# Kernel optimization log

Measured on AMD Instinct MI355X. Metric: run time of the kernel, lower is better.

## Reference

```python
import jax, jax.numpy as jnp
import numpy as np


def _cal_similarity(query, respond):
    # query: [B, n1, d], respond: [B, n2, d]
    # scores[b, c, q, r] = <query[b, q], respond[c, r]>
    scores = jnp.einsum('bqd,crd->bcqr', query, respond)  # [B, B, n1, n2]
    # max over respond tokens, mean over query tokens -> [B, B]
    return scores.max(axis=-1).mean(axis=-1)


def _ce_with_arange_labels(logits):
    # cross-entropy with labels = arange(B), mean reduction
    logp = jax.nn.log_softmax(logits, axis=-1)
    return -jnp.mean(jnp.diagonal(logp))


def setup_inputs() -> dict:
    key = jax.random.key(0)
    k1, k2 = jax.random.split(key)
    B, n1, n2, d = 96, 196, 77, 512
    image_out = jax.random.normal(k1, (B, n1, d), dtype=jnp.float32)
    text_out = jax.random.normal(k2, (B, n2, d), dtype=jnp.float32)
    return {"image_out": image_out, "text_out": text_out}


def reference(image_out, text_out):
    i2t = _cal_similarity(image_out, text_out)  # [B, B]
    t2i = _cal_similarity(text_out, image_out)  # [B, B]
    return 0.5 * (_ce_with_arange_labels(i2t) + _ce_with_arange_labels(t2i))
```

## Files before the change

kernel.cpp:

```cpp
#include <hip/hip_runtime.h>
#include <math.h>

#define BB 96
#define N1 196
#define N2 77
#define DD 512

#define IMGN (BB * N1 * DD)
#define TXTN (BB * N2 * DD)

#define ATILES 13
#define NTILES 24
#define BUFH (NTILES * 512)

typedef _Float16 f16x8 __attribute__((ext_vector_type(8)));
typedef float f4v __attribute__((ext_vector_type(4)));

typedef unsigned int __attribute__((address_space(1))) as1_uint;
typedef unsigned int __attribute__((address_space(3))) as3_uint;

__device__ __forceinline__ void gload_lds16(const void* g, void* l) {
    __builtin_amdgcn_global_load_lds((const as1_uint*)g, (as3_uint*)l, 16, 0, 0);
}

__global__ void convert_kernel(const float* __restrict__ img,
                               const float* __restrict__ txt,
                               _Float16* __restrict__ dst) {
    int i = (blockIdx.x * blockDim.x + threadIdx.x) * 4;
    if (i >= IMGN + TXTN) return;
    const float* src = (i < IMGN) ? (img + i) : (txt + (i - IMGN));
    float4 v = *(const float4*)src;
    union { _Float16 h[4]; uint2 u; } o;
    o.h[0] = (_Float16)v.x; o.h[1] = (_Float16)v.y;
    o.h[2] = (_Float16)v.z; o.h[3] = (_Float16)v.w;
    *(uint2*)(dst + i) = o.u;
}

template <int SG0, int NS, int H>
__device__ __forceinline__ void compute_sub(const f16x8* __restrict__ fr,
                                            f4v* __restrict__ acc, int lane) {
    f16x8 b[5];
#pragma unroll
    for (int ct = 0; ct < 5; ++ct)
        b[ct] = fr[(ATILES + H * 5 + ct) * 64 + lane];
#pragma unroll
    for (int i = 0; i < NS; ++i) {
        f16x8 a = fr[(SG0 + i) * 64 + lane];
#pragma unroll
        for (int ct = 0; ct < 5; ++ct)
            acc[i * 5 + ct] = __builtin_amdgcn_mfma_f32_16x16x32_f16(
                a, b[ct], acc[i * 5 + ct], 0, 0, 0);
    }
}

template <int SG0, int NS, int H>
__device__ __forceinline__ void reduce_phase1(const f4v* __restrict__ acc,
                                              int g, int lq, int lm,
                                              float* __restrict__ rp,
                                              float* __restrict__ cp) {
    float colm[5];
#pragma unroll
    for (int ct = 0; ct < 5; ++ct) colm[ct] = -INFINITY;
#pragma unroll
    for (int i = 0; i < NS; ++i) {
        const int s = SG0 + i;
        float rowm[4] = {-INFINITY, -INFINITY, -INFINITY, -INFINITY};
        bool rows_ok = (s != 12) || (lq == 0);
#pragma unroll
        for (int ct = 0; ct < 5; ++ct) {
            f4v a = acc[i * 5 + ct];
            bool col_ok = (ct != 4) || (lm < N2 - 64);
            float cm = fmaxf(fmaxf(a[0], a[1]), fmaxf(a[2], a[3]));
            colm[ct] = fmaxf(colm[ct], rows_ok ? cm : -INFINITY);
#pragma unroll
            for (int r = 0; r < 4; ++r)
                rowm[r] = fmaxf(rowm[r], col_ok ? a[r] : -INFINITY);
        }
#pragma unroll
        for (int r = 0; r < 4; ++r) {
            float m = rowm[r];
            m = fmaxf(m, __shfl_xor(m, 1));
            m = fmaxf(m, __shfl_xor(m, 2));
            m = fmaxf(m, __shfl_xor(m, 4));
            m = fmaxf(m, __shfl_xor(m, 8));
            if (lm == 0) rp[H * 208 + s * 16 + lq * 4 + r] = m;
        }
    }
#pragma unroll
    for (int ct = 0; ct < 5; ++ct) {
        float m = colm[ct];
        m = fmaxf(m, __shfl_xor(m, 16));
        m = fmaxf(m, __shfl_xor(m, 32));
        if (lq == 0) cp[g * 160 + H * 80 + ct * 16 + lm] = m;
    }
}

template <bool PRE>
__global__ __launch_bounds__(256, 2) void sim_mfma_kernel(
    const float* __restrict__ imgF, const float* __restrict__ txtF,
    const _Float16* __restrict__ h16,
    float* __restrict__ i2t, float* __restrict__ t2i)
{
    const int id  = blockIdx.x;
    const int xcd = id & 7;
    const int lid = id >> 3;
    const int w   = lid % 48;
    const int btq = lid / 48;
    const int btp = btq * 4 + (w & 3);
    const int bi  = xcd * 12 + (w >> 2);
    const int bt0 = btp * 2;

    const int tid = threadIdx.x;
    const int wave = tid >> 6, lane = tid & 63;
    const int lm = lane & 15;
    const int lq = lane >> 4;
    const int g = wave >> 1;

    __shared__ __align__(16) _Float16 lds[3 * BUFH];
    float* scratch = (float*)(lds + 2 * BUFH);
    float* rp   = scratch;
    float* cp   = scratch + 416;
    float* sws  = scratch + 736;
    float* scol = scratch + 740;

    int off[6];
    const float* fsrc[6];
#pragma unroll
    for (int j = 0; j < 6; ++j) {
        const int T = 4 * j + wave;
        int o;
        bool isA = true;
        if (T < ATILES) {
            int q = T * 16 + lm; q = q > (N1 - 1) ? (N1 - 1) : q;
            o = (bi * N1 + q) * DD + lq * 8;
        } else if (T < 23) {
            isA = false;
            int ct = T - ATILES;
            int bt = bt0 + (ct >= 5);
            int r = (ct % 5) * 16 + lm; r = r > (N2 - 1) ? (N2 - 1) : r;
            o = (bt * N2 + r) * DD + lq * 8;
        } else {
            o = lq * 8;
        }
        if constexpr (PRE) {
            off[j] = isA ? o : (IMGN + o);
        } else {
            off[j] = o;
            fsrc[j] = isA ? imgF : txtF;
        }
    }

    auto stage = [&](int kc, int b) {
        const int k0 = kc * 32;
#pragma unroll
        for (int j = 0; j < 6; ++j)
            gload_lds16(h16 + off[j] + k0,
                        lds + (b * NTILES + 4 * j + wave) * 512);
    };

    f4v acc[35];
#pragma unroll
    for (int i = 0; i < 35; ++i) acc[i] = (f4v){0.f, 0.f, 0.f, 0.f};

    auto do_compute = [&](const f16x8* fr) {
        if (wave == 0)      compute_sub<0, 7, 0>(fr, acc, lane);
        else if (wave == 1) compute_sub<0, 7, 1>(fr, acc, lane);
        else if (wave == 2) compute_sub<7, 6, 0>(fr, acc, lane);
        else                compute_sub<7, 6, 1>(fr, acc, lane);
    };

    if constexpr (PRE) {
        stage(0, 0);
        stage(1, 1);
#pragma unroll 1
        for (int kc = 0; kc < 16; ++kc) {
            if (kc < 14) {
                stage(kc + 2, (kc + 2) % 3);
                asm volatile("s_waitcnt vmcnt(12)" ::: "memory");
            } else if (kc == 14) {
                asm volatile("s_waitcnt vmcnt(6)" ::: "memory");
            } else {
                asm volatile("s_waitcnt vmcnt(0)" ::: "memory");
            }
            __builtin_amdgcn_s_barrier();
            asm volatile("" ::: "memory");
            do_compute((const f16x8*)(lds + (kc % 3) * BUFH));
            asm volatile("" ::: "memory");
            __builtin_amdgcn_s_barrier();
        }
    } else {
#pragma unroll 1
        for (int kc = 0; kc < 16; ++kc) {
            __syncthreads();
            const int k0 = kc * 32;
#pragma unroll
            for (int j = 0; j < 6; ++j) {
                const int T = 4 * j + wave;
                if (T < 23) {
                    float4 v0 = *(const float4*)(fsrc[j] + off[j] + k0);
                    float4 v1 = *(const float4*)(fsrc[j] + off[j] + k0 + 4);
                    union { f16x8 f; uint4 u; } o;
                    o.f[0] = (_Float16)v0.x; o.f[1] = (_Float16)v0.y;
                    o.f[2] = (_Float16)v0.z; o.f[3] = (_Float16)v0.w;
                    o.f[4] = (_Float16)v1.x; o.f[5] = (_Float16)v1.y;
                    o.f[6] = (_Float16)v1.z; o.f[7] = (_Float16)v1.w;
                    ((uint4*)lds)[T * 64 + lane] = o.u;
                }
            }
            __syncthreads();
            do_compute((const f16x8*)lds);
        }
        __syncthreads();
    }

    if (wave == 0)      reduce_phase1<0, 7, 0>(acc, g, lq, lm, rp, cp);
    else if (wave == 1) reduce_phase1<0, 7, 1>(acc, g, lq, lm, rp, cp);
    else if (wave == 2) reduce_phase1<7, 6, 0>(acc, g, lq, lm, rp, cp);
    else                reduce_phase1<7, 6, 1>(acc, g, lq, lm, rp, cp);
    __syncthreads();

    {
        const int h = wave & 1;
        const int sseg = wave >> 1;
        const int qa = sseg * 128 + lane;
        const int qb = qa + 64;
        float v = rp[h * 208 + qa];
        if (qb < N1) v += rp[h * 208 + qb];
        v += __shfl_xor(v, 1);  v += __shfl_xor(v, 2);  v += __shfl_xor(v, 4);
        v += __shfl_xor(v, 8);  v += __shfl_xor(v, 16); v += __shfl_xor(v, 32);
        if (lane == 0) sws[wave] = v;
    }
    if (tid < 160) scol[tid] = fmaxf(cp[tid], cp[160 + tid]);
    __syncthreads();
    if (tid == 0)
        i2t[bi * BB + bt0] = (sws[0] + sws[2]) * (1.f / (float)N1);
    if (tid == 1)
        i2t[bi * BB + bt0 + 1] = (sws[1] + sws[3]) * (1.f / (float)N1);
    if (wave < 2) {
        const float* c = scol + wave * 80;
        float cv = c[lane] + ((lane < N2 - 64) ? c[64 + lane] : 0.f);
        cv += __shfl_xor(cv, 1);  cv += __shfl_xor(cv, 2);  cv += __shfl_xor(cv, 4);
        cv += __shfl_xor(cv, 8);  cv += __shfl_xor(cv, 16); cv += __shfl_xor(cv, 32);
        if (lane == 0)
            t2i[(bt0 + wave) * BB + bi] = cv * (1.f / (float)N2);
    }
}

__global__ __launch_bounds__(256) void ce_kernel(
    const float* __restrict__ i2t, const float* __restrict__ t2i,
    float* __restrict__ out)
{
    const int tid = threadIdx.x;
    const int wid = tid >> 6;
    const int lane = tid & 63;

    float contrib = 0.f;
    if (tid < 2 * BB) {
        const float* M = (tid < BB) ? i2t : t2i;
        const int b = (tid < BB) ? tid : tid - BB;
        const float* row = M + b * BB;
        float mx = row[0];
#pragma unroll 1
        for (int c = 1; c < BB; ++c) mx = fmaxf(mx, row[c]);
        float s = 0.f;
#pragma unroll 1
        for (int c = 0; c < BB; ++c) s += expf(row[c] - mx);
        float lse = mx + logf(s);
        contrib = row[b] - lse;
    }
    contrib += __shfl_xor(contrib, 1);
    contrib += __shfl_xor(contrib, 2);
    contrib += __shfl_xor(contrib, 4);
    contrib += __shfl_xor(contrib, 8);
    contrib += __shfl_xor(contrib, 16);
    contrib += __shfl_xor(contrib, 32);

    __shared__ float s_part[4];
    if (lane == 0) s_part[wid] = contrib;
    __syncthreads();
    if (tid == 0) {
        float total = s_part[0] + s_part[1] + s_part[2] + s_part[3];
        out[0] = -total * (1.f / (float)(2 * BB));
    }
}

extern "C" void kernel_launch(void* const* d_in, const int* in_sizes, int n_in,
                              void* d_out, int out_size, void* d_ws, size_t ws_size,
                              hipStream_t stream) {
    const float* img = (const float*)d_in[0];
    const float* txt = (const float*)d_in[1];
    float* i2t = (float*)d_ws;
    float* t2i = i2t + BB * BB;

    const size_t conv_off = 2 * BB * BB * sizeof(float);
    const size_t need = conv_off + (size_t)(IMGN + TXTN) * sizeof(_Float16);

    const int nblocks = BB * (BB / 2);
    if (ws_size >= need) {
        _Float16* h16 = (_Float16*)((char*)d_ws + conv_off);
        const int ntot = (IMGN + TXTN) / 4;
        convert_kernel<<<(ntot + 255) / 256, 256, 0, stream>>>(img, txt, h16);
        sim_mfma_kernel<true><<<nblocks, 256, 0, stream>>>(img, txt, h16, i2t, t2i);
    } else {
        sim_mfma_kernel<false><<<nblocks, 256, 0, stream>>>(img, txt, nullptr, i2t, t2i);
    }
    ce_kernel<<<1, 256, 0, stream>>>(i2t, t2i, (float*)d_out);
}
```

Baseline: 306.2 us.

## Replace LDS-direct triple buffering with register-staged double buffering and split compute

Replaces the global_load_lds triple-buffered pipeline with a double-buffered scheme where tiles are loaded into registers two steps ahead and written to LDS mid-compute, between front and tail halves of the MFMA work. It drops the unused 24th tile slot, reduces LDS footprint (scratch now aliases the buffer), and raises wave priority during MFMA sections. The goal is to lower LDS use for occupancy and to interleave memory traffic with math. The cost is extra VGPRs for staging, which risks register pressure with the 35 accumulators. Scratch aliasing buffer 0 also relies on the final barrier before the reduction.

```diff
diff --git a/kernel.cpp b/kernel.cpp
--- a/kernel.cpp
+++ b/kernel.cpp
@@ -10,18 +10,11 @@
 #define TXTN (BB * N2 * DD)
 
 #define ATILES 13
-#define NTILES 24
+#define NTILES 23
 #define BUFH (NTILES * 512)
 
 typedef _Float16 f16x8 __attribute__((ext_vector_type(8)));
 typedef float f4v __attribute__((ext_vector_type(4)));
-
-typedef unsigned int __attribute__((address_space(1))) as1_uint;
-typedef unsigned int __attribute__((address_space(3))) as3_uint;
-
-__device__ __forceinline__ void gload_lds16(const void* g, void* l) {
-    __builtin_amdgcn_global_load_lds((const as1_uint*)g, (as3_uint*)l, 16, 0, 0);
-}
 
 __global__ void convert_kernel(const float* __restrict__ img,
                                const float* __restrict__ txt,
@@ -116,8 +109,8 @@
     const int lq = lane >> 4;
     const int g = wave >> 1;
 
-    __shared__ __align__(16) _Float16 lds[3 * BUFH];
-    float* scratch = (float*)(lds + 2 * BUFH);
+    __shared__ __align__(16) _Float16 lds[2 * BUFH];
+    float* scratch = (float*)lds;
     float* rp   = scratch;
     float* cp   = scratch + 416;
     float* sws  = scratch + 736;
@@ -150,43 +143,62 @@
         }
     }
 
-    auto stage = [&](int kc, int b) {
-        const int k0 = kc * 32;
-#pragma unroll
-        for (int j = 0; j < 6; ++j)
-            gload_lds16(h16 + off[j] + k0,
-                        lds + (b * NTILES + 4 * j + wave) * 512);
+    f4v acc[35];
+#pragma unroll
+    for (int i = 0; i < 35; ++i) acc[i] = (f4v){0.f, 0.f, 0.f, 0.f};
+
+    auto compute_front = [&](const f16x8* fr) {
+        if (wave == 0)      compute_sub<0, 4, 0>(fr, acc, lane);
+        else if (wave == 1) compute_sub<0, 4, 1>(fr, acc, lane);
+        else if (wave == 2) compute_sub<7, 3, 0>(fr, acc, lane);
+        else                compute_sub<7, 3, 1>(fr, acc, lane);
     };
-
-    f4v acc[35];
-#pragma unroll
-    for (int i = 0; i < 35; ++i) acc[i] = (f4v){0.f, 0.f, 0.f, 0.f};
-
-    auto do_compute = [&](const f16x8* fr) {
-        if (wave == 0)      compute_sub<0, 7, 0>(fr, acc, lane);
-        else if (wave == 1) compute_sub<0, 7, 1>(fr, acc, lane);
-        else if (wave == 2) compute_sub<7, 6, 0>(fr, acc, lane);
-        else                compute_sub<7, 6, 1>(fr, acc, lane);
+    auto compute_tail = [&](const f16x8* fr) {
+        if (wave == 0)      compute_sub<4, 3, 0>(fr, acc + 20, lane);
+        else if (wave == 1) compute_sub<4, 3, 1>(fr, acc + 20, lane);
+        else if (wave == 2) compute_sub<10, 3, 0>(fr, acc + 15, lane);
+        else                compute_sub<10, 3, 1>(fr, acc + 15, lane);
     };
 
     if constexpr (PRE) {
-        stage(0, 0);
-        stage(1, 1);
+        const uint4* gq[6];
+#pragma unroll
+        for (int j = 0; j < 6; ++j) gq[j] = (const uint4*)(h16 + off[j]);
+
+        uint4 st[6];
+        auto reg_load = [&](int kc) {
+            const int k4 = kc * 4;
+#pragma unroll
+            for (int j = 0; j < 6; ++j)
+                if (4 * j + wave < 23) st[j] = gq[j][k4];
+        };
+        auto lds_write = [&](int b) {
+#pragma unroll
+            for (int j = 0; j < 6; ++j)
+                if (4 * j + wave < 23)
+                    ((uint4*)lds)[(b * NTILES + 4 * j + wave) * 64 + lane]
+                        = st[j];
+        };
+
+        reg_load(0);
+        lds_write(0);
+        reg_load(1);
+        __syncthreads();
 #pragma unroll 1
         for (int kc = 0; kc < 16; ++kc) {
-            if (kc < 14) {
-                stage(kc + 2, (kc + 2) % 3);
-                asm volatile("s_waitcnt vmcnt(12)" ::: "memory");
-            } else if (kc == 14) {
-                asm volatile("s_waitcnt vmcnt(6)" ::: "memory");
-            } else {
-                asm volatile("s_waitcnt vmcnt(0)" ::: "memory");
-            }
-            __builtin_amdgcn_s_barrier();
+            const f16x8* fr = (const f16x8*)(lds + (kc & 1) * BUFH);
+            __builtin_amdgcn_s_setprio(1);
+            compute_front(fr);
+            __builtin_amdgcn_s_setprio(0);
             asm volatile("" ::: "memory");
-            do_compute((const f16x8*)(lds + (kc % 3) * BUFH));
+            if (kc + 1 < 16) lds_write((kc + 1) & 1);
             asm volatile("" ::: "memory");
-            __builtin_amdgcn_s_barrier();
+            if (kc + 2 < 16) reg_load(kc + 2);
+            asm volatile("" ::: "memory");
+            __builtin_amdgcn_s_setprio(1);
+            compute_tail(fr);
+            __builtin_amdgcn_s_setprio(0);
+            __syncthreads();
         }
     } else {
 #pragma unroll 1
@@ -208,7 +220,8 @@
                 }
             }
             __syncthreads();
-            do_compute((const f16x8*)lds);
+            compute_front((const f16x8*)lds);
+            compute_tail((const f16x8*)lds);
         }
         __syncthreads();
     }
```

Measured after the change: 679.8 us. +122.0%, slower.

## Pre-tile fp16 conversion into MFMA-fragment order for contiguous LDS staging

Applied to the files above, without the earlier changes.

The fp32-to-fp16 conversion kernel now writes its output in a tiled layout. Each 16-row by 32-k fragment is stored as a contiguous 1 KB block, with rows padded by clamping. The similarity kernel then stages each fragment with fully contiguous 16-byte-per-lane global_load_lds reads instead of strided row reads. This targets memory coalescing in the main GEMM-like kernel, at the cost of an LDS transpose pass and slightly larger workspace in the conversion kernel.

```diff
diff --git a/kernel.cpp b/kernel.cpp
--- a/kernel.cpp
+++ b/kernel.cpp
@@ -13,6 +13,14 @@
 #define NTILES 24
 #define BUFH (NTILES * 512)
 
+#define TA_TILES (BB * 13 * 16)
+#define TB_TILES (BB * 5 * 16)
+#define NT_TILES (TA_TILES + TB_TILES)
+
+#define NSTRIPS_A (BB * 13)
+#define NSTRIPS_B (BB * 5)
+#define NSTRIPS   (NSTRIPS_A + NSTRIPS_B)
+
 typedef _Float16 f16x8 __attribute__((ext_vector_type(8)));
 typedef float f4v __attribute__((ext_vector_type(4)));
 
@@ -23,17 +31,49 @@
     __builtin_amdgcn_global_load_lds((const as1_uint*)g, (as3_uint*)l, 16, 0, 0);
 }
 
-__global__ void convert_kernel(const float* __restrict__ img,
-                               const float* __restrict__ txt,
-                               _Float16* __restrict__ dst) {
-    int i = (blockIdx.x * blockDim.x + threadIdx.x) * 4;
-    if (i >= IMGN + TXTN) return;
-    const float* src = (i < IMGN) ? (img + i) : (txt + (i - IMGN));
-    float4 v = *(const float4*)src;
-    union { _Float16 h[4]; uint2 u; } o;
-    o.h[0] = (_Float16)v.x; o.h[1] = (_Float16)v.y;
-    o.h[2] = (_Float16)v.z; o.h[3] = (_Float16)v.w;
-    *(uint2*)(dst + i) = o.u;
+__global__ __launch_bounds__(256) void convert_tiled_kernel(
+    const float* __restrict__ img, const float* __restrict__ txt,
+    _Float16* __restrict__ dst)
+{
+    __shared__ _Float16 sh[16 * 520];
+    const int sid = blockIdx.x;
+    const int tid = threadIdx.x;
+    const float* base;
+    int rowbase, rmax, tile0;
+    if (sid < NSTRIPS_A) {
+        const int bi = sid / 13, s = sid % 13;
+        base = img + (size_t)bi * N1 * DD;
+        rowbase = s * 16; rmax = N1 - 1;
+        tile0 = sid * 16;
+    } else {
+        const int bs = sid - NSTRIPS_A;
+        const int bt = bs / 5, ct = bs % 5;
+        base = txt + (size_t)bt * N2 * DD;
+        rowbase = ct * 16; rmax = N2 - 1;
+        tile0 = TA_TILES + bs * 16;
+    }
+#pragma unroll
+    for (int it = 0; it < 8; ++it) {
+        const int u  = it * 256 + tid;
+        const int r  = u >> 7;
+        const int c4 = u & 127;
+        int q = rowbase + r; q = q > rmax ? rmax : q;
+        float4 v = *(const float4*)(base + (size_t)q * DD + c4 * 4);
+        union { _Float16 h[4]; uint2 u2; } o;
+        o.h[0] = (_Float16)v.x; o.h[1] = (_Float16)v.y;
+        o.h[2] = (_Float16)v.z; o.h[3] = (_Float16)v.w;
+        *(uint2*)(sh + r * 520 + c4 * 4) = o.u2;
+    }
+    __syncthreads();
+#pragma unroll
+    for (int it = 0; it < 4; ++it) {
+        const int w  = it * 256 + tid;
+        const int kc = w >> 6;
+        const int c  = w & 63;
+        const int r16 = c & 15, k8 = c >> 4;
+        uint4 val = *(const uint4*)(sh + r16 * 520 + kc * 32 + k8 * 8);
+        *(uint4*)(dst + (size_t)(tile0 + kc) * 512 + c * 8) = val;
+    }
 }
 
 template <int SG0, int NS, int H>
@@ -128,30 +168,40 @@
 #pragma unroll
     for (int j = 0; j < 6; ++j) {
         const int T = 4 * j + wave;
-        int o;
-        bool isA = true;
-        if (T < ATILES) {
-            int q = T * 16 + lm; q = q > (N1 - 1) ? (N1 - 1) : q;
-            o = (bi * N1 + q) * DD + lq * 8;
-        } else if (T < 23) {
-            isA = false;
-            int ct = T - ATILES;
-            int bt = bt0 + (ct >= 5);
-            int r = (ct % 5) * 16 + lm; r = r > (N2 - 1) ? (N2 - 1) : r;
-            o = (bt * N2 + r) * DD + lq * 8;
+        if constexpr (PRE) {
+            int t;
+            if (T < ATILES) {
+                t = (bi * 13 + T) * 16;
+            } else if (T < 23) {
+                const int ct = T - ATILES;
+                const int bt = bt0 + (ct >= 5);
+                t = TA_TILES + (bt * 5 + (ct % 5)) * 16;
+            } else {
+                t = 0;
+            }
+            off[j] = t * 512 + lane * 8;
         } else {
-            o = lq * 8;
-        }
-        if constexpr (PRE) {
-            off[j] = isA ? o : (IMGN + o);
-        } else {
+            int o;
+            bool isA = true;
+            if (T < ATILES) {
+                int q = T * 16 + lm; q = q > (N1 - 1) ? (N1 - 1) : q;
+                o = (bi * N1 + q) * DD + lq * 8;
+            } else if (T < 23) {
+                isA = false;
+                int ct = T - ATILES;
+                int bt = bt0 + (ct >= 5);
+                int r = (ct % 5) * 16 + lm; r = r > (N2 - 1) ? (N2 - 1) : r;
+                o = (bt * N2 + r) * DD + lq * 8;
+            } else {
+                o = lq * 8;
+            }
             off[j] = o;
             fsrc[j] = isA ? imgF : txtF;
         }
     }
 
     auto stage = [&](int kc, int b) {
-        const int k0 = kc * 32;
+        const int k0 = kc * 512;
 #pragma unroll
         for (int j = 0; j < 6; ++j)
             gload_lds16(h16 + off[j] + k0,
@@ -293,13 +343,12 @@
     float* t2i = i2t + BB * BB;
 
     const size_t conv_off = 2 * BB * BB * sizeof(float);
-    const size_t need = conv_off + (size_t)(IMGN + TXTN) * sizeof(_Float16);
+    const size_t need = conv_off + (size_t)NT_TILES * 512 * sizeof(_Float16);
 
     const int nblocks = BB * (BB / 2);
     if (ws_size >= need) {
         _Float16* h16 = (_Float16*)((char*)d_ws + conv_off);
-        const int ntot = (IMGN + TXTN) / 4;
-        convert_kernel<<<(ntot + 255) / 256, 256, 0, stream>>>(img, txt, h16);
+        convert_tiled_kernel<<<NSTRIPS, 256, 0, stream>>>(img, txt, h16);
         sim_mfma_kernel<true><<<nblocks, 256, 0, stream>>>(img, txt, h16, i2t, t2i);
     } else {
         sim_mfma_kernel<false><<<nblocks, 256, 0, stream>>>(img, txt, nullptr, i2t, t2i);
```

Result: no change. 309.4 us (+1.0%).
